# Kernel tuning notes

Measured on AMD Instinct MI355X. Metric: run time of the kernel, lower is better.

Reference implementation:

```python
import jax, jax.numpy as jnp
import numpy as np

# Module hyperparameters (init_kwargs defaults)
FOV_RATIO = 0.3125
K_RATIO = 0.208
SALIENCY_BETA = 0.5

B, C, H, W = 32, 3, 512, 512


def setup_inputs() -> dict:
    key = jax.random.key(0)
    k1, k2, k3 = jax.random.split(key, 3)
    img = jax.random.uniform(k1, (B, C, H, W), jnp.float32) * 255.0  # uint8-range pixels
    gaze = jax.random.uniform(k2, (B, 2), jnp.float32) * (min(H, W) - 1)  # (x, y) inside image
    saliency = jax.random.uniform(k3, (B, 1, H, W), jnp.float32)
    return {"img": img, "gaze": gaze, "saliency": saliency}


def _bilinear_grid_sample(img, grid):
    # img: (B,C,H,W) float; grid: (B,H,W,2) normalized coords in [-1,1]
    # Matches F.grid_sample(mode='bilinear', padding_mode='zeros', align_corners=True)
    Bh, Ch, Hh, Wh = img.shape
    x = (grid[..., 0] + 1.0) * 0.5 * (Wh - 1)  # (B,H,W) pixel coords
    y = (grid[..., 1] + 1.0) * 0.5 * (Hh - 1)
    x0 = jnp.floor(x)
    y0 = jnp.floor(y)
    x1 = x0 + 1.0
    y1 = y0 + 1.0
    wx1 = x - x0
    wx0 = 1.0 - wx1
    wy1 = y - y0
    wy0 = 1.0 - wy1

    def gather_one(im, yi, xi):
        # im: (C,H,W); yi, xi: (H,W) float corner coords
        valid = (xi >= 0) & (xi <= Wh - 1) & (yi >= 0) & (yi <= Hh - 1)
        xc = jnp.clip(xi, 0, Wh - 1).astype(jnp.int32)
        yc = jnp.clip(yi, 0, Hh - 1).astype(jnp.int32)
        vals = im[:, yc, xc]  # (C,H,W)
        return vals * valid[None].astype(im.dtype)

    gather = jax.vmap(gather_one)
    v00 = gather(img, y0, x0)
    v01 = gather(img, y0, x1)
    v10 = gather(img, y1, x0)
    v11 = gather(img, y1, x1)
    w00 = (wy0 * wx0)[:, None]
    w01 = (wy0 * wx1)[:, None]
    w10 = (wy1 * wx0)[:, None]
    w11 = (wy1 * wx1)[:, None]
    return v00 * w00 + v01 * w01 + v10 * w10 + v11 * w11


def _forward_float(img, gaze, saliency):
    Bh, Ch, Hh, Wh = img.shape
    ys = jnp.arange(Hh, dtype=img.dtype)[None, :, None]  # (1,H,1)
    xs = jnp.arange(Wh, dtype=img.dtype)[None, None, :]  # (1,1,W)
    x_g = gaze[:, 0][:, None, None]  # (B,1,1)
    y_g = gaze[:, 1][:, None, None]
    dx = xs - x_g  # (B,H,W)
    dy = ys - y_g
    r = jnp.sqrt(dx * dx + dy * dy + 1e-6)

    S = saliency[:, 0]  # (B,H,W)
    S = S / (S.sum(axis=(1, 2), keepdims=True) + 1e-6)
    mean_r = jnp.sum(S * r, axis=(1, 2), keepdims=True)
    mean_r2 = jnp.sum(S * r * r, axis=(1, 2), keepdims=True)
    var_r = mean_r2 - mean_r * mean_r
    std_r = jnp.sqrt(jnp.clip(var_r, 0.0, None))
    r_max = r.max(axis=(1, 2), keepdims=True)
    spread_norm = std_r / r_max  # (B,1,1)

    base_size = min(Hh, Wh)
    fov = FOV_RATIO * base_size
    K = K_RATIO * base_size
    fov_eff = fov * (1.0 + SALIENCY_BETA * spread_norm)  # (B,1,1)

    # radial_quadratic_batch, branchless
    r_peri = (r + K) ** 2 / (2.0 * (fov_eff + K)) + (fov_eff - K) / 2.0
    r_tfm = jnp.where(r < fov_eff, r, r_peri)
    coef = r_max / (r_tfm.max(axis=(1, 2), keepdims=True) + 1e-6)
    r_new = coef * r_tfm

    dx_norm = dx / r
    dy_norm = dy / r
    X_new = x_g + dx_norm * r_new
    Y_new = y_g + dy_norm * r_new
    X_norm = X_new / (Wh - 1) * 2.0 - 1.0
    Y_norm = Y_new / (Hh - 1) * 2.0 - 1.0
    grid = jnp.stack((X_norm, Y_norm), axis=-1)  # (B,H,W,2)
    out = _bilinear_grid_sample(img, grid)
    return jnp.clip(out, 0.0, 255.0)


def reference(img, gaze, saliency):
    return _forward_float(img, gaze, saliency).astype(jnp.uint8)
```

## Files before the change

kernel.cpp:

```cpp
#include <hip/hip_runtime.h>

#define Bn 32
#define Cn 3
#define Hn 512
#define Wn 512
#define HWn (Hn * Wn)

#define FOVc 160.0f
#define Kc   106.496f

__global__ __launch_bounds__(256) void reduce_k(const float4* __restrict__ sal,
                                                const float* __restrict__ gaze,
                                                float* __restrict__ ws) {
    const int b = blockIdx.y;
    const float xg = gaze[2 * b + 0];
    const float yg = gaze[2 * b + 1];
    const int tid = threadIdx.x;
    const int idx0 = blockIdx.x * 256 + tid;
    const float4* sb = sal + (size_t)b * (HWn / 4);

    float sumS = 0.0f, sumSr = 0.0f, sumSr2 = 0.0f, rmax = 0.0f;

    for (int i = idx0; i < HWn / 4; i += 16 * 256) {
        float4 s4 = sb[i];
        const int pix = i * 4;
        const float y = (float)(pix >> 9);
        const float xbase = (float)(pix & 511);
        const float dy = y - yg;
        const float dy2 = dy * dy + 1e-6f;
        const float sv[4] = {s4.x, s4.y, s4.z, s4.w};
#pragma unroll
        for (int j = 0; j < 4; ++j) {
            const float dx = xbase + (float)j - xg;
            const float r = sqrtf(dx * dx + dy2);
            const float s = sv[j];
            sumS   += s;
            sumSr  += s * r;
            sumSr2 += s * r * r;
            rmax = fmaxf(rmax, r);
        }
    }

#pragma unroll
    for (int off = 32; off > 0; off >>= 1) {
        sumS   += __shfl_down(sumS, off);
        sumSr  += __shfl_down(sumSr, off);
        sumSr2 += __shfl_down(sumSr2, off);
        rmax = fmaxf(rmax, __shfl_down(rmax, off));
    }

    __shared__ float red[4][4];
    const int wave = tid >> 6, lane = tid & 63;
    if (lane == 0) {
        red[wave][0] = sumS; red[wave][1] = sumSr; red[wave][2] = sumSr2; red[wave][3] = rmax;
    }
    __syncthreads();
    if (tid == 0) {
        float a = 0, c = 0, d = 0, m = 0;
        for (int w = 0; w < 4; ++w) {
            a += red[w][0]; c += red[w][1]; d += red[w][2]; m = fmaxf(m, red[w][3]);
        }
        atomicAdd(&ws[b * 4 + 0], a);
        atomicAdd(&ws[b * 4 + 1], c);
        atomicAdd(&ws[b * 4 + 2], d);
        atomicMax(reinterpret_cast<int*>(&ws[b * 4 + 3]), __float_as_int(m));
    }
}

__global__ void finalize_k(float* __restrict__ ws) {
    const int b = threadIdx.x;
    if (b >= Bn) return;
    const float sumS   = ws[b * 4 + 0];
    const float sumSr  = ws[b * 4 + 1];
    const float sumSr2 = ws[b * 4 + 2];
    const float rmax   = ws[b * 4 + 3];

    const float inv = 1.0f / (sumS + 1e-6f);
    const float mean_r  = sumSr * inv;
    const float mean_r2 = sumSr2 * inv;
    const float var_r = mean_r2 - mean_r * mean_r;
    const float std_r = sqrtf(fmaxf(var_r, 0.0f));
    const float spread = std_r / rmax;
    const float fov_eff = FOVc * (1.0f + 0.5f * spread);

    float t;
    if (rmax < fov_eff) {
        t = rmax;
    } else {
        const float rk = rmax + Kc;
        t = rk * rk / (2.0f * (fov_eff + Kc)) + (fov_eff - Kc) * 0.5f;
    }
    const float coef = rmax / (t + 1e-6f);

    ws[128 + b] = fov_eff;
    ws[160 + b] = coef;
}

__global__ __launch_bounds__(256) void sample_k(const float* __restrict__ img,
                                                const float* __restrict__ gaze,
                                                const float* __restrict__ ws,
                                                int* __restrict__ out) {
    const int b = blockIdx.y;
    const int pix = blockIdx.x * 256 + threadIdx.x;

    const float xg = gaze[2 * b + 0];
    const float yg = gaze[2 * b + 1];
    const float fov_eff = ws[128 + b];
    const float coef    = ws[160 + b];

    const float y = (float)(pix >> 9);
    const float x = (float)(pix & 511);
    const float dx = x - xg;
    const float dy = y - yg;
    const float r = sqrtf(dx * dx + dy * dy + 1e-6f);

    const float rk = r + Kc;
    const float r_peri = rk * rk / (2.0f * (fov_eff + Kc)) + (fov_eff - Kc) * 0.5f;
    const float r_tfm = (r < fov_eff) ? r : r_peri;
    const float r_new = coef * r_tfm;
    const float scale = r_new / r;

    const float X = xg + dx * scale;
    const float Y = yg + dy * scale;

    const float x0f = floorf(X), y0f = floorf(Y);
    const float x1f = x0f + 1.0f, y1f = y0f + 1.0f;
    const float wx1 = X - x0f, wx0 = 1.0f - wx1;
    const float wy1 = Y - y0f, wy0 = 1.0f - wy1;

    const float m00 = (x0f >= 0.0f && x0f <= 511.0f && y0f >= 0.0f && y0f <= 511.0f) ? 1.0f : 0.0f;
    const float m01 = (x1f >= 0.0f && x1f <= 511.0f && y0f >= 0.0f && y0f <= 511.0f) ? 1.0f : 0.0f;
    const float m10 = (x0f >= 0.0f && x0f <= 511.0f && y1f >= 0.0f && y1f <= 511.0f) ? 1.0f : 0.0f;
    const float m11 = (x1f >= 0.0f && x1f <= 511.0f && y1f >= 0.0f && y1f <= 511.0f) ? 1.0f : 0.0f;

    const int xi0 = (int)fminf(fmaxf(x0f, 0.0f), 511.0f);
    const int xi1 = (int)fminf(fmaxf(x1f, 0.0f), 511.0f);
    const int yi0 = (int)fminf(fmaxf(y0f, 0.0f), 511.0f);
    const int yi1 = (int)fminf(fmaxf(y1f, 0.0f), 511.0f);

    const float w00 = wy0 * wx0 * m00;
    const float w01 = wy0 * wx1 * m01;
    const float w10 = wy1 * wx0 * m10;
    const float w11 = wy1 * wx1 * m11;

    const int o00 = yi0 * Wn + xi0;
    const int o01 = yi0 * Wn + xi1;
    const int o10 = yi1 * Wn + xi0;
    const int o11 = yi1 * Wn + xi1;

    const float* ib = img + (size_t)b * Cn * HWn;
#pragma unroll
    for (int c = 0; c < Cn; ++c) {
        const float* p = ib + (size_t)c * HWn;
        float v = p[o00] * w00 + p[o01] * w01 + p[o10] * w10 + p[o11] * w11;
        v = fminf(fmaxf(v, 0.0f), 255.0f);
        out[((size_t)b * Cn + c) * HWn + pix] = (int)v;
    }
}

extern "C" void kernel_launch(void* const* d_in, const int* in_sizes, int n_in,
                              void* d_out, int out_size, void* d_ws, size_t ws_size,
                              hipStream_t stream) {
    const float* img  = (const float*)d_in[0];
    const float* gaze = (const float*)d_in[1];
    const float* sal  = (const float*)d_in[2];
    int* out  = (int*)d_out;
    float* ws = (float*)d_ws;

    hipMemsetAsync(d_ws, 0, 128 * sizeof(float), stream);

    reduce_k<<<dim3(16, Bn), 256, 0, stream>>>((const float4*)sal, gaze, ws);
    finalize_k<<<1, 32, 0, stream>>>(ws);
    sample_k<<<dim3(HWn / 256, Bn), 256, 0, stream>>>(img, gaze, ws, out);
}
```

Before: 241.8 us.

## Fold finalize into sample kernel, process four pixels per thread, widen reduction grid

Removes the single-block finalize kernel by recomputing the per-batch fov_eff and coef inside each sample block from the reduction workspace, which saves one launch and its serialization. Each sample thread now handles four consecutive pixels and writes them with one int4 store, and the radius uses rsq to avoid sqrt and divides. The reduction grid doubles to 32 blocks per image for more parallelism, at the cost of more atomics. The trade-off is redundant scalar math per block, more registers per thread, and a small change in rounding from the rsq approximation.

```diff
diff --git a/kernel.cpp b/kernel.cpp
--- a/kernel.cpp
+++ b/kernel.cpp
@@ -21,7 +21,7 @@
 
     float sumS = 0.0f, sumSr = 0.0f, sumSr2 = 0.0f, rmax = 0.0f;
 
-    for (int i = idx0; i < HWn / 4; i += 16 * 256) {
+    for (int i = idx0; i < HWn / 4; i += 32 * 256) {
         float4 s4 = sb[i];
         const int pix = i * 4;
         const float y = (float)(pix >> 9);
@@ -67,94 +67,100 @@
     }
 }
 
-__global__ void finalize_k(float* __restrict__ ws) {
-    const int b = threadIdx.x;
-    if (b >= Bn) return;
-    const float sumS   = ws[b * 4 + 0];
-    const float sumSr  = ws[b * 4 + 1];
-    const float sumSr2 = ws[b * 4 + 2];
-    const float rmax   = ws[b * 4 + 3];
-
-    const float inv = 1.0f / (sumS + 1e-6f);
-    const float mean_r  = sumSr * inv;
-    const float mean_r2 = sumSr2 * inv;
-    const float var_r = mean_r2 - mean_r * mean_r;
-    const float std_r = sqrtf(fmaxf(var_r, 0.0f));
-    const float spread = std_r / rmax;
-    const float fov_eff = FOVc * (1.0f + 0.5f * spread);
-
-    float t;
-    if (rmax < fov_eff) {
-        t = rmax;
-    } else {
-        const float rk = rmax + Kc;
-        t = rk * rk / (2.0f * (fov_eff + Kc)) + (fov_eff - Kc) * 0.5f;
-    }
-    const float coef = rmax / (t + 1e-6f);
-
-    ws[128 + b] = fov_eff;
-    ws[160 + b] = coef;
-}
-
 __global__ __launch_bounds__(256) void sample_k(const float* __restrict__ img,
                                                 const float* __restrict__ gaze,
                                                 const float* __restrict__ ws,
                                                 int* __restrict__ out) {
     const int b = blockIdx.y;
-    const int pix = blockIdx.x * 256 + threadIdx.x;
+    const int pix0 = (blockIdx.x * 256 + threadIdx.x) * 4;
 
     const float xg = gaze[2 * b + 0];
     const float yg = gaze[2 * b + 1];
-    const float fov_eff = ws[128 + b];
-    const float coef    = ws[160 + b];
 
-    const float y = (float)(pix >> 9);
-    const float x = (float)(pix & 511);
-    const float dx = x - xg;
+    const float sumS   = ws[b * 4 + 0];
+    const float sumSr  = ws[b * 4 + 1];
+    const float sumSr2 = ws[b * 4 + 2];
+    const float rmax   = ws[b * 4 + 3];
+    const float inv = 1.0f / (sumS + 1e-6f);
+    const float mean_r  = sumSr * inv;
+    const float mean_r2 = sumSr2 * inv;
+    const float var_r = fmaxf(mean_r2 - mean_r * mean_r, 0.0f);
+    const float spread = sqrtf(var_r) / rmax;
+    const float fov_eff = FOVc * (1.0f + 0.5f * spread);
+    float tmax;
+    if (rmax < fov_eff) {
+        tmax = rmax;
+    } else {
+        const float rk = rmax + Kc;
+        tmax = rk * rk / (2.0f * (fov_eff + Kc)) + (fov_eff - Kc) * 0.5f;
+    }
+    const float coef = rmax / (tmax + 1e-6f);
+    const float inv2fk = 0.5f / (fov_eff + Kc);
+    const float addc   = (fov_eff - Kc) * 0.5f;
+
+    const float y  = (float)(pix0 >> 9);
+    const float xb = (float)(pix0 & 511);
     const float dy = y - yg;
-    const float r = sqrtf(dx * dx + dy * dy + 1e-6f);
+    const float dy2 = dy * dy + 1e-6f;
 
-    const float rk = r + Kc;
-    const float r_peri = rk * rk / (2.0f * (fov_eff + Kc)) + (fov_eff - Kc) * 0.5f;
-    const float r_tfm = (r < fov_eff) ? r : r_peri;
-    const float r_new = coef * r_tfm;
-    const float scale = r_new / r;
+    float w00[4], w01[4], w10[4], w11[4];
+    int   o00[4], o01[4], o10[4], o11[4];
 
-    const float X = xg + dx * scale;
-    const float Y = yg + dy * scale;
+#pragma unroll
+    for (int j = 0; j < 4; ++j) {
+        const float dx = xb + (float)j - xg;
+        const float d2 = dx * dx + dy2;
+        const float inv_r = __builtin_amdgcn_rsqf(d2);
+        const float r = d2 * inv_r;
 
-    const float x0f = floorf(X), y0f = floorf(Y);
-    const float x1f = x0f + 1.0f, y1f = y0f + 1.0f;
-    const float wx1 = X - x0f, wx0 = 1.0f - wx1;
-    const float wy1 = Y - y0f, wy0 = 1.0f - wy1;
+        const float rk = r + Kc;
+        const float r_peri = rk * rk * inv2fk + addc;
+        const float r_tfm = (r < fov_eff) ? r : r_peri;
+        const float scale = coef * r_tfm * inv_r;
 
-    const float m00 = (x0f >= 0.0f && x0f <= 511.0f && y0f >= 0.0f && y0f <= 511.0f) ? 1.0f : 0.0f;
-    const float m01 = (x1f >= 0.0f && x1f <= 511.0f && y0f >= 0.0f && y0f <= 511.0f) ? 1.0f : 0.0f;
-    const float m10 = (x0f >= 0.0f && x0f <= 511.0f && y1f >= 0.0f && y1f <= 511.0f) ? 1.0f : 0.0f;
-    const float m11 = (x1f >= 0.0f && x1f <= 511.0f && y1f >= 0.0f && y1f <= 511.0f) ? 1.0f : 0.0f;
+        const float X = xg + dx * scale;
+        const float Y = yg + dy * scale;
 
-    const int xi0 = (int)fminf(fmaxf(x0f, 0.0f), 511.0f);
-    const int xi1 = (int)fminf(fmaxf(x1f, 0.0f), 511.0f);
-    const int yi0 = (int)fminf(fmaxf(y0f, 0.0f), 511.0f);
-    const int yi1 = (int)fminf(fmaxf(y1f, 0.0f), 511.0f);
+        const float x0f = floorf(X), y0f = floorf(Y);
+        const float x1f = x0f + 1.0f, y1f = y0f + 1.0f;
+        const float wx1 = X - x0f, wx0 = 1.0f - wx1;
+        const float wy1 = Y - y0f, wy0 = 1.0f - wy1;
 
-    const float w00 = wy0 * wx0 * m00;
-    const float w01 = wy0 * wx1 * m01;
-    const float w10 = wy1 * wx0 * m10;
-    const float w11 = wy1 * wx1 * m11;
+        const bool vx0 = (x0f >= 0.0f) & (x0f <= 511.0f);
+        const bool vx1 = (x1f >= 0.0f) & (x1f <= 511.0f);
+        const bool vy0 = (y0f >= 0.0f) & (y0f <= 511.0f);
+        const bool vy1 = (y1f >= 0.0f) & (y1f <= 511.0f);
 
-    const int o00 = yi0 * Wn + xi0;
-    const int o01 = yi0 * Wn + xi1;
-    const int o10 = yi1 * Wn + xi0;
-    const int o11 = yi1 * Wn + xi1;
+        const int xi0 = (int)fminf(fmaxf(x0f, 0.0f), 511.0f);
+        const int xi1 = (int)fminf(fmaxf(x1f, 0.0f), 511.0f);
+        const int yi0 = (int)fminf(fmaxf(y0f, 0.0f), 511.0f);
+        const int yi1 = (int)fminf(fmaxf(y1f, 0.0f), 511.0f);
+
+        w00[j] = wy0 * wx0 * ((vy0 & vx0) ? 1.0f : 0.0f);
+        w01[j] = wy0 * wx1 * ((vy0 & vx1) ? 1.0f : 0.0f);
+        w10[j] = wy1 * wx0 * ((vy1 & vx0) ? 1.0f : 0.0f);
+        w11[j] = wy1 * wx1 * ((vy1 & vx1) ? 1.0f : 0.0f);
+
+        o00[j] = yi0 * Wn + xi0;
+        o01[j] = yi0 * Wn + xi1;
+        o10[j] = yi1 * Wn + xi0;
+        o11[j] = yi1 * Wn + xi1;
+    }
 
     const float* ib = img + (size_t)b * Cn * HWn;
 #pragma unroll
     for (int c = 0; c < Cn; ++c) {
         const float* p = ib + (size_t)c * HWn;
-        float v = p[o00] * w00 + p[o01] * w01 + p[o10] * w10 + p[o11] * w11;
-        v = fminf(fmaxf(v, 0.0f), 255.0f);
-        out[((size_t)b * Cn + c) * HWn + pix] = (int)v;
+        int4 res;
+        float v0 = p[o00[0]] * w00[0] + p[o01[0]] * w01[0] + p[o10[0]] * w10[0] + p[o11[0]] * w11[0];
+        float v1 = p[o00[1]] * w00[1] + p[o01[1]] * w01[1] + p[o10[1]] * w10[1] + p[o11[1]] * w11[1];
+        float v2 = p[o00[2]] * w00[2] + p[o01[2]] * w01[2] + p[o10[2]] * w10[2] + p[o11[2]] * w11[2];
+        float v3 = p[o00[3]] * w00[3] + p[o01[3]] * w01[3] + p[o10[3]] * w10[3] + p[o11[3]] * w11[3];
+        res.x = (int)fminf(fmaxf(v0, 0.0f), 255.0f);
+        res.y = (int)fminf(fmaxf(v1, 0.0f), 255.0f);
+        res.z = (int)fminf(fmaxf(v2, 0.0f), 255.0f);
+        res.w = (int)fminf(fmaxf(v3, 0.0f), 255.0f);
+        *reinterpret_cast<int4*>(&out[((size_t)b * Cn + c) * HWn + pix0]) = res;
     }
 }
 
@@ -169,7 +175,6 @@
 
     hipMemsetAsync(d_ws, 0, 128 * sizeof(float), stream);
 
-    reduce_k<<<dim3(16, Bn), 256, 0, stream>>>((const float4*)sal, gaze, ws);
-    finalize_k<<<1, 32, 0, stream>>>(ws);
-    sample_k<<<dim3(HWn / 256, Bn), 256, 0, stream>>>(img, gaze, ws, out);
+    reduce_k<<<dim3(32, Bn), 256, 0, stream>>>((const float4*)sal, gaze, ws);
+    sample_k<<<dim3(HWn / 1024, Bn), 256, 0, stream>>>(img, gaze, ws, out);
 }
```

Result: slower. 276.8 us (+14.5%).
